# Optimization experiments

Hardware: AMD Instinct MI355X
Metric: run time of the kernel (lower is better)

The kernel has to match this reference:

```python
import jax, jax.numpy as jnp
import numpy as np

CLASS_DIM = 4   # hardcoded in DsFunction1
PROTO_DIM = 20  # hardcoded in DsFunction1


def setup_inputs() -> dict:
    key = jax.random.key(0)
    k1, k2, k3 = jax.random.split(key, 3)
    B, C, H, Wd, D = 2, 16, 64, 64, 64
    inp = jax.random.normal(k1, (B, C, H, Wd, D), dtype=jnp.float32)
    W = jax.random.normal(k2, (PROTO_DIM, C), dtype=jnp.float32)
    BETA = jax.random.normal(k3, (PROTO_DIM, CLASS_DIM), dtype=jnp.float32) * 0.5
    alpha = jnp.zeros((PROTO_DIM, 1), dtype=jnp.float32)           # init 0 per reset_parameters
    gamma = jnp.full((PROTO_DIM, 1), 0.1, dtype=jnp.float32)       # init 0.1 per reset_parameters
    return {"input": inp, "W": W, "BETA": BETA, "alpha": alpha, "gamma": gamma}


def _ds_forward(x, W, BETA, alpha, gamma):
    # x: [B,C,H,Wd,D]; W: [K,C]; BETA: [K,M]; alpha, gamma: [K,1]
    B, C, H, Wd, D = x.shape
    BETA2 = BETA * BETA
    U = BETA2 / jnp.sum(BETA2, axis=1, keepdims=True)              # [K,M] membership weights
    alphap = 0.99 / (1.0 + jnp.exp(-alpha[:, 0]))                  # [K]

    # squared distances to prototypes: d[k] = 0.5 * ||x - W_k||^2 over channel dim
    x2 = jnp.sum(x * x, axis=1)                                    # [B,H,Wd,D]
    xw = jnp.einsum('bchwd,kc->kbhwd', x, W)                       # [K,B,H,Wd,D]
    w2 = jnp.sum(W * W, axis=1)                                    # [K]
    d = 0.5 * (x2[None] - 2.0 * xw + w2[:, None, None, None, None])  # [K,B,H,Wd,D]

    g2 = (gamma[:, 0] ** 2)[:, None, None, None, None]
    s = alphap[:, None, None, None, None] * jnp.exp(-g2 * d)       # [K,B,H,Wd,D]

    mfoc = U[:, :, None, None, None, None] * s[:, None]            # [K,M,B,H,Wd,D] focal masses
    momega = 1.0 - s                                               # [K,B,H,Wd,D] mass on Omega

    # sequential Dempster (unnormalized conjunctive) combination over prototypes
    def step(carry, km):
        mk_f, mk_o = carry                                         # [M,B,H,Wd,D], [B,H,Wd,D]
        m_f, m_o = km
        new_f = mk_f * (m_f + m_o[None]) + m_f * mk_o[None]
        new_o = mk_o * m_o
        return (new_f, new_o), None

    init = (jnp.zeros((CLASS_DIM, B, H, Wd, D), x.dtype),
            jnp.ones((B, H, Wd, D), x.dtype))
    (mk_f, mk_o), _ = jax.lax.scan(step, init, (mfoc, momega))

    mk = jnp.concatenate([mk_f, mk_o[None]], axis=0)               # [M+1,B,H,Wd,D]
    mk_n = mk / jnp.sum(mk, axis=0, keepdims=True)                 # normalize masses
    return jnp.transpose(mk_n, (1, 0, 2, 3, 4))                    # [B,M+1,H,Wd,D]


def reference(input, W, BETA, alpha, gamma):
    return _ds_forward(input, W, BETA, alpha, gamma)
```

## Files before the change

kernel.cpp:

```cpp
#include <hip/hip_runtime.h>
#include <hip/hip_bf16.h>
#include <math.h>

#define NK 20
#define NC 16
#define NM 4
#define TSTEP 4

typedef __attribute__((ext_vector_type(8)))  short  short8;
typedef __attribute__((ext_vector_type(16))) float  floatx16;

static __device__ __forceinline__ short bf16b(float f) {
    __hip_bfloat16 h = __float2bfloat16(f);
    return *reinterpret_cast<short*>(&h);
}

__global__ __launch_bounds__(256, 4) void ds_fused(
    const float* __restrict__ inp,
    const float* __restrict__ Wg,
    const float* __restrict__ BETAg,
    const float* __restrict__ alphag,
    const float* __restrict__ gammag,
    float* __restrict__ out,
    int S,
    int BS)
{
    __shared__ __align__(16) float sCst[32][8];
    __shared__ __align__(16) short sWpb[32][16];
    __shared__ short sA2[32][2];

    const int t    = threadIdx.x;
    const int lane = t & 63;
    const int half = lane >> 5;
    const int col  = lane & 31;

    const int ebase = (blockIdx.x * 4 + (t >> 6)) * (TSTEP * 32);
    const int b     = (ebase >= S) ? 1 : 0;
    const int spw   = ebase - b * S;
    const float* xb = inp + (size_t)b * NC * S + spw + col;

    float xv[TSTEP][8];
    #pragma unroll
    for (int tt = 0; tt < TSTEP; ++tt)
        #pragma unroll
        for (int j = 0; j < 8; ++j)
            xv[tt][j] = xb[(size_t)(8*half + j) * S + tt*32];

    if (t < 32) {
        if (t < NK) {
            const float L   = 1.4426950408889634f;
            const float g   = gammag[t];
            const float g2L = g * g * L;
            float w2 = 0.f;
            #pragma unroll
            for (int c = 0; c < NC; ++c) {
                const float wv = Wg[t*NC + c];
                sWpb[t][c] = bf16b(g2L * wv);
                w2 = fmaf(wv, wv, w2);
            }
            const float a = 0.99f / (1.0f + __expf(-alphag[t]));
            float b0 = BETAg[t*NM+0], b1 = BETAg[t*NM+1], b2 = BETAg[t*NM+2], b3 = BETAg[t*NM+3];
            b0 *= b0; b1 *= b1; b2 *= b2; b3 *= b3;
            const float uinv = 1.0f / (b0 + b1 + b2 + b3);
            sCst[t][0] = (1.0f - b0*uinv) * a;
            sCst[t][1] = (1.0f - b1*uinv) * a;
            sCst[t][2] = (1.0f - b2*uinv) * a;
            sCst[t][3] = (1.0f - b3*uinv) * a;
            sCst[t][4] = a;
            sCst[t][5] = 0.f; sCst[t][6] = 0.f; sCst[t][7] = 0.f;
            sA2[t][0] = bf16b(-0.5f * g2L);
            sA2[t][1] = bf16b(-0.5f * g2L * w2);
        } else {
            #pragma unroll
            for (int i = 0; i < 8; ++i) sCst[t][i] = 0.f;
            #pragma unroll
            for (int c = 0; c < NC; ++c) sWpb[t][c] = 0;
            sA2[t][0] = 0; sA2[t][1] = 0;
        }
    }
    __syncthreads();

    const short8 afrag = *(const short8*)&sWpb[col][half*8];
    short8 a2frag;
    #pragma unroll
    for (int j = 0; j < 8; ++j) a2frag[j] = 0;
    if (half == 0) { a2frag[0] = sA2[col][0]; a2frag[1] = sA2[col][1]; }

    float4 cm[12];
    #pragma unroll
    for (int r = 0; r < 12; ++r) {
        const int p = (r & 3) + 8*(r >> 2) + 4*half;
        cm[r] = *(const float4*)&sCst[p][0];
    }

    short8 b2base;
    #pragma unroll
    for (int j = 0; j < 8; ++j) b2base[j] = 0;
    if (half == 0) b2base[1] = (short)0x3F80;

    float* ob = out + (size_t)b * (NM+1) * S + spw + col;

    #pragma unroll
    for (int tt = 0; tt < TSTEP; ++tt) {
        short8 bfrag;
        float x2p = 0.f;
        #pragma unroll
        for (int j = 0; j < 8; ++j) {
            const float v = xv[tt][j];
            x2p = fmaf(v, v, x2p);
            bfrag[j] = bf16b(v);
        }
        const float x2 = x2p + __shfl_xor(x2p, 32, 64);

        short8 b2frag = b2base;
        if (half == 0) b2frag[0] = bf16b(x2);

        floatx16 acc;
        #pragma unroll
        for (int i = 0; i < 16; ++i) acc[i] = 0.f;
        acc = __builtin_amdgcn_mfma_f32_32x32x16_bf16(afrag,  bfrag,  acc, 0, 0, 0);
        acc = __builtin_amdgcn_mfma_f32_32x32x16_bf16(a2frag, b2frag, acc, 0, 0, 0);

        float P0 = 1.f, P1 = 1.f, P2 = 1.f, P3 = 1.f, PO = 1.f;
        #pragma unroll
        for (int r = 0; r < 12; ++r) {
            const float ek = __builtin_amdgcn_exp2f(acc[r]);
            const float cO = (cm[r].x + cm[r].y + cm[r].z + cm[r].w) * (1.0f/3.0f);
            P0 *= fmaf(-cm[r].x, ek, 1.0f);
            P1 *= fmaf(-cm[r].y, ek, 1.0f);
            P2 *= fmaf(-cm[r].z, ek, 1.0f);
            P3 *= fmaf(-cm[r].w, ek, 1.0f);
            PO *= fmaf(-cO,      ek, 1.0f);
        }
        P0 *= __shfl_xor(P0, 32, 64);
        P1 *= __shfl_xor(P1, 32, 64);
        P2 *= __shfl_xor(P2, 32, 64);
        P3 *= __shfl_xor(P3, 32, 64);
        PO *= __shfl_xor(PO, 32, 64);

        const float O  = PO;
        const float f0 = P0 - O, f1 = P1 - O, f2 = P2 - O, f3 = P3 - O;
        const float inv = 1.0f / (f0 + f1 + f2 + f3 + O);

        float* op = ob + tt*32;
        if (half == 0) {
            op[0]           = f0 * inv;
            op[(size_t)S]   = f1 * inv;
            op[(size_t)2*S] = f2 * inv;
        } else {
            op[(size_t)3*S] = f3 * inv;
            op[(size_t)4*S] = O  * inv;
        }
    }
}

extern "C" void kernel_launch(void* const* d_in, const int* in_sizes, int n_in,
                              void* d_out, int out_size, void* d_ws, size_t ws_size,
                              hipStream_t stream) {
    const float* inp   = (const float*)d_in[0];
    const float* Wg    = (const float*)d_in[1];
    const float* BETAg = (const float*)d_in[2];
    const float* alphag= (const float*)d_in[3];
    const float* gammag= (const float*)d_in[4];
    float* out = (float*)d_out;

    const int BS = in_sizes[0] / NC;
    const int S  = BS / 2;

    const int grid = BS / 512;
    ds_fused<<<grid, 256, 0, stream>>>(inp, Wg, BETAg, alphag, gammag, out, S, BS);
}
```

Baseline: 87.43 us.

## Pack per-prototype constants as half2 and halve per-wave work for occupancy

```diff
diff --git a/kernel.cpp b/kernel.cpp
--- a/kernel.cpp
+++ b/kernel.cpp
@@ -1,11 +1,12 @@
 #include <hip/hip_runtime.h>
 #include <hip/hip_bf16.h>
+#include <hip/hip_fp16.h>
 #include <math.h>
 
 #define NK 20
 #define NC 16
 #define NM 4
-#define TSTEP 4
+#define TSTEP 2
 
 typedef __attribute__((ext_vector_type(8)))  short  short8;
 typedef __attribute__((ext_vector_type(16))) float  floatx16;
@@ -15,7 +16,7 @@
     return *reinterpret_cast<short*>(&h);
 }
 
-__global__ __launch_bounds__(256, 4) void ds_fused(
+__global__ __launch_bounds__(256, 6) void ds_fused(
     const float* __restrict__ inp,
     const float* __restrict__ Wg,
     const float* __restrict__ BETAg,
@@ -25,9 +26,10 @@
     int S,
     int BS)
 {
-    __shared__ __align__(16) float sCst[32][8];
     __shared__ __align__(16) short sWpb[32][16];
-    __shared__ short sA2[32][2];
+    __shared__ short   sA2[32][2];
+    __shared__ __half2 sPkA[32];
+    __shared__ __half2 sPkB[32];
 
     const int t    = threadIdx.x;
     const int lane = t & 63;
@@ -62,19 +64,15 @@
             float b0 = BETAg[t*NM+0], b1 = BETAg[t*NM+1], b2 = BETAg[t*NM+2], b3 = BETAg[t*NM+3];
             b0 *= b0; b1 *= b1; b2 *= b2; b3 *= b3;
             const float uinv = 1.0f / (b0 + b1 + b2 + b3);
-            sCst[t][0] = (1.0f - b0*uinv) * a;
-            sCst[t][1] = (1.0f - b1*uinv) * a;
-            sCst[t][2] = (1.0f - b2*uinv) * a;
-            sCst[t][3] = (1.0f - b3*uinv) * a;
-            sCst[t][4] = a;
-            sCst[t][5] = 0.f; sCst[t][6] = 0.f; sCst[t][7] = 0.f;
+            sPkA[t] = __floats2half2_rn((1.0f - b0*uinv) * a, (1.0f - b1*uinv) * a);
+            sPkB[t] = __floats2half2_rn((1.0f - b2*uinv) * a, (1.0f - b3*uinv) * a);
             sA2[t][0] = bf16b(-0.5f * g2L);
             sA2[t][1] = bf16b(-0.5f * g2L * w2);
         } else {
             #pragma unroll
-            for (int i = 0; i < 8; ++i) sCst[t][i] = 0.f;
-            #pragma unroll
             for (int c = 0; c < NC; ++c) sWpb[t][c] = 0;
+            sPkA[t] = __floats2half2_rn(0.f, 0.f);
+            sPkB[t] = __floats2half2_rn(0.f, 0.f);
             sA2[t][0] = 0; sA2[t][1] = 0;
         }
     }
@@ -86,17 +84,13 @@
     for (int j = 0; j < 8; ++j) a2frag[j] = 0;
     if (half == 0) { a2frag[0] = sA2[col][0]; a2frag[1] = sA2[col][1]; }
 
-    float4 cm[12];
+    __half2 cmA[12], cmB[12];
     #pragma unroll
     for (int r = 0; r < 12; ++r) {
         const int p = (r & 3) + 8*(r >> 2) + 4*half;
-        cm[r] = *(const float4*)&sCst[p][0];
+        cmA[r] = sPkA[p];
+        cmB[r] = sPkB[p];
     }
-
-    short8 b2base;
-    #pragma unroll
-    for (int j = 0; j < 8; ++j) b2base[j] = 0;
-    if (half == 0) b2base[1] = (short)0x3F80;
 
     float* ob = out + (size_t)b * (NM+1) * S + spw + col;
 
@@ -112,8 +106,10 @@
         }
         const float x2 = x2p + __shfl_xor(x2p, 32, 64);
 
-        short8 b2frag = b2base;
-        if (half == 0) b2frag[0] = bf16b(x2);
+        short8 b2frag;
+        #pragma unroll
+        for (int j = 0; j < 8; ++j) b2frag[j] = 0;
+        if (half == 0) { b2frag[0] = bf16b(x2); b2frag[1] = (short)0x3F80; }
 
         floatx16 acc;
         #pragma unroll
@@ -125,12 +121,14 @@
         #pragma unroll
         for (int r = 0; r < 12; ++r) {
             const float ek = __builtin_amdgcn_exp2f(acc[r]);
-            const float cO = (cm[r].x + cm[r].y + cm[r].z + cm[r].w) * (1.0f/3.0f);
-            P0 *= fmaf(-cm[r].x, ek, 1.0f);
-            P1 *= fmaf(-cm[r].y, ek, 1.0f);
-            P2 *= fmaf(-cm[r].z, ek, 1.0f);
-            P3 *= fmaf(-cm[r].w, ek, 1.0f);
-            PO *= fmaf(-cO,      ek, 1.0f);
+            const float2 cab = __half22float2(cmA[r]);
+            const float2 ccd = __half22float2(cmB[r]);
+            const float cO = (cab.x + cab.y + ccd.x + ccd.y) * (1.0f/3.0f);
+            P0 *= fmaf(-cab.x, ek, 1.0f);
+            P1 *= fmaf(-cab.y, ek, 1.0f);
+            P2 *= fmaf(-ccd.x, ek, 1.0f);
+            P3 *= fmaf(-ccd.y, ek, 1.0f);
+            PO *= fmaf(-cO,    ek, 1.0f);
         }
         P0 *= __shfl_xor(P0, 32, 64);
         P1 *= __shfl_xor(P1, 32, 64);
@@ -167,6 +165,6 @@
     const int BS = in_sizes[0] / NC;
     const int S  = BS / 2;
 
-    const int grid = BS / 512;
+    const int grid = BS / 256;
     ds_fused<<<grid, 256, 0, stream>>>(inp, Wg, BETAg, alphag, gammag, out, S, BS);
 }
```

Result: slower. 99.91 us (+14.3%).
